# Performance work log

Measured on AMD Instinct MI355X. Metric: run time of the kernel, lower is better.

## Reference

```python
import jax, jax.numpy as jnp
import numpy as np

B = 131072
NF, E = 9, 8
D0 = NF * E  # 72
H = 64       # expert hidden
O = 8        # expert output
T, SE, SH = 3, 3, 3
VOCAB = 160000

PARAM_SHAPES = {
    "emb_table": (VOCAB, E),
    "spec0_W1": (T, SE, D0, H), "spec0_b1": (T, SE, H),
    "spec0_W2": (T, SE, H, O),  "spec0_b2": (T, SE, O),
    "shar0_W1": (SH, D0, H),    "shar0_b1": (SH, H),
    "shar0_W2": (SH, H, O),     "shar0_b2": (SH, O),
    "gate0_W1": (T, D0, H),     "gate0_b1": (T, H),
    "gate0_W2": (T, H, O),      "gate0_b2": (T, O),
    "gate0_W3": (T, O, SE + SH),
    "sgate0_W1": (D0, H), "sgate0_b1": (H,),
    "sgate0_W2": (H, O),  "sgate0_b2": (O,),
    "sgate0_W3": (O, T * SE + SH),
    "spec1_W1": (T, SE, O, H), "spec1_b1": (T, SE, H),
    "spec1_W2": (T, SE, H, O), "spec1_b2": (T, SE, O),
    "shar1_W1": (SH, O, H),    "shar1_b1": (SH, H),
    "shar1_W2": (SH, H, O),    "shar1_b2": (SH, O),
    "gate1_W1": (T, O, H),     "gate1_b1": (T, H),
    "gate1_W2": (T, H, O),     "gate1_b2": (T, O),
    "gate1_W3": (T, O, SE + SH),
    "tower_W": (T, O, 1), "tower_b": (T, 1),
}


def setup_inputs() -> dict:
    key = jax.random.key(0)
    keys = jax.random.split(key, len(PARAM_SHAPES) + 1)
    inp = {n: jax.random.normal(k, s, jnp.float32) * 0.1
           for (n, s), k in zip(PARAM_SHAPES.items(), keys[:-1])}
    inp["cat_idx"] = jax.random.randint(keys[-1], (B, NF), 0, VOCAB, jnp.int32)
    return inp


def _cgc(task_x, shared_x, sW1, sb1, sW2, sb2, hW1, hb1, hW2, hb2,
         gW1, gb1, gW2, gb2, gW3, sgate=None):
    """One CGC level. task_x: [T,B,in], shared_x: [B,in]."""
    # task-specific experts, batched over (task, expert)
    h = jax.nn.relu(jnp.einsum('tbi,teih->tebh', task_x, sW1) + sb1[:, :, None, :])
    spec = jax.nn.relu(jnp.einsum('tebh,teho->tebo', h, sW2) + sb2[:, :, None, :])  # [T,SE,B,O]
    # shared experts, batched over expert
    hs = jax.nn.relu(jnp.einsum('bi,eih->ebh', shared_x, hW1) + hb1[:, None, :])
    shar = jax.nn.relu(jnp.einsum('ebh,eho->ebo', hs, hW2) + hb2[:, None, :])       # [SH,B,O]
    # per-task gates: MLP[64,8] relu -> linear(no bias) -> softmax over SE+SH experts
    g = jax.nn.relu(jnp.einsum('tbi,tih->tbh', task_x, gW1) + gb1[:, None, :])
    g = jax.nn.relu(jnp.einsum('tbh,tho->tbo', g, gW2) + gb2[:, None, :])
    gw = jax.nn.softmax(jnp.einsum('tbo,toe->tbe', g, gW3), axis=-1)                # [T,B,SE+SH]
    experts = jnp.concatenate(
        [spec, jnp.broadcast_to(shar[None], (spec.shape[0],) + shar.shape)], axis=1)  # [T,SE+SH,B,O]
    task_out = jnp.einsum('tebo,tbe->tbo', experts, gw)                             # [T,B,O]
    if sgate is None:
        return task_out, None
    sgW1, sgb1, sgW2, sgb2, sgW3 = sgate
    gs = jax.nn.relu(shared_x @ sgW1 + sgb1)
    gs = jax.nn.relu(gs @ sgW2 + sgb2)
    gws = jax.nn.softmax(gs @ sgW3, axis=-1)                                        # [B,T*SE+SH]
    all_e = jnp.concatenate([spec.reshape(T * SE, spec.shape[2], O), shar], axis=0)  # [T*SE+SH,B,O]
    shared_out = jnp.einsum('ebo,be->bo', all_e, gws)
    return task_out, shared_out


def _forward(cat_idx, p):
    x = p["emb_table"][cat_idx].reshape(cat_idx.shape[0], -1)  # [B, 72]
    task_x = jnp.broadcast_to(x[None], (T,) + x.shape)
    task_x, shared_x = _cgc(
        task_x, x,
        p["spec0_W1"], p["spec0_b1"], p["spec0_W2"], p["spec0_b2"],
        p["shar0_W1"], p["shar0_b1"], p["shar0_W2"], p["shar0_b2"],
        p["gate0_W1"], p["gate0_b1"], p["gate0_W2"], p["gate0_b2"], p["gate0_W3"],
        sgate=(p["sgate0_W1"], p["sgate0_b1"], p["sgate0_W2"], p["sgate0_b2"], p["sgate0_W3"]))
    task_x, _ = _cgc(
        task_x, shared_x,
        p["spec1_W1"], p["spec1_b1"], p["spec1_W2"], p["spec1_b2"],
        p["shar1_W1"], p["shar1_b1"], p["shar1_W2"], p["shar1_b2"],
        p["gate1_W1"], p["gate1_b1"], p["gate1_W2"], p["gate1_b2"], p["gate1_W3"],
        sgate=None)
    # 3 sigmoid towers -> stacked [T, B, 1] (== dict task_0..task_2 in original)
    out = jax.nn.sigmoid(jnp.einsum('tbo,tok->tbk', task_x, p["tower_W"]) + p["tower_b"][:, None, :])
    return out


def reference(cat_idx, emb_table, spec0_W1, spec0_b1, spec0_W2, spec0_b2,
              shar0_W1, shar0_b1, shar0_W2, shar0_b2,
              gate0_W1, gate0_b1, gate0_W2, gate0_b2, gate0_W3,
              sgate0_W1, sgate0_b1, sgate0_W2, sgate0_b2, sgate0_W3,
              spec1_W1, spec1_b1, spec1_W2, spec1_b2,
              shar1_W1, shar1_b1, shar1_W2, shar1_b2,
              gate1_W1, gate1_b1, gate1_W2, gate1_b2, gate1_W3,
              tower_W, tower_b):
    p = dict(locals())
    p.pop('cat_idx')
    return _forward(cat_idx, p)
```

## Files before the change

### kernel.cpp

```cpp
#include <hip/hip_runtime.h>


#define NT 256
#define EPB 64

typedef unsigned short u16;
typedef unsigned int u32;
typedef __fp16 hv2 __attribute__((ext_vector_type(2)));
typedef __fp16 half8 __attribute__((ext_vector_type(8)));
typedef __attribute__((ext_vector_type(4))) float floatx4;

__device__ __forceinline__ u32 pkh2(float a, float b){
  hv2 v = __builtin_amdgcn_cvt_pkrtz(a, b);
  u32 r; __builtin_memcpy(&r, &v, 4); return r;
}
__device__ __forceinline__ u16 f2h(float a){
  __fp16 h = (__fp16)a; u16 r; __builtin_memcpy(&r, &h, 2); return r;
}
__device__ __forceinline__ float h2f(u16 v){
  __fp16 h; __builtin_memcpy(&h, &v, 2); return (float)h;
}
__device__ __forceinline__ float dot2(u32 a, u32 b, float c){
  hv2 av, bv; __builtin_memcpy(&av, &a, 4); __builtin_memcpy(&bv, &b, 4);
  return __builtin_amdgcn_fdot2(av, bv, c, false);
}

#define W1F0 0
#define W2F0 49152
#define W1F1 57344
#define W2F1 72704
#define OFF_b1P0 80384
#define OFF_b2P0 81408
#define OFF_b1P1 81664
#define OFF_b2P1 82624
#define OFF_G0W3 82864
#define OFF_SG0W3 83008
#define OFF_G1W3 83104
#define OFF_TW   83248
#define OFF_Tb   83272
#define CVT_TOTAL 83275

struct PSrc { const float* p[33]; };

__global__ void cvt_kernel(PSrc S, u32* __restrict__ wsU, float* __restrict__ wsF){
  int i = blockIdx.x*256 + threadIdx.x;
  if (i >= CVT_TOTAL) return;
  if (i < 49152){
    int j2 = i & 3, l = (i>>2)&63, tt = (i>>8)&3;
    int rest = i >> 10; int s = rest % 3, u = rest / 3;
    int k0 = s*32 + (l>>4)*8 + 2*j2;
    int h  = tt*16 + (l&15);
    const float* src = (u<9)  ? S.p[0]  + (u*72)*64
                     : (u<12) ? S.p[4]  + ((u-9)*72)*64
                     : (u<15) ? S.p[8]  + ((u-12)*72)*64
                              : S.p[13];
    float lo = (k0   < 72) ? src[(k0  )*64 + h] : 0.f;
    float hi = (k0+1 < 72) ? src[(k0+1)*64 + h] : 0.f;
    wsU[i] = pkh2(lo, hi);
    return;
  }
  i -= 49152;
  if (i < 8192){
    int j2 = i & 3, l = (i>>2)&63, ks = (i>>8)&1, u = i>>9;
    int q = l >> 4, n = l & 15;
    int h0 = (2*ks + ((2*j2)>>2))*16 + q*4 + ((2*j2)&3);
    const float* src = (u<9)  ? S.p[2]  + u*512
                     : (u<12) ? S.p[6]  + (u-9)*512
                     : (u<15) ? S.p[10] + (u-12)*512
                              : S.p[15];
    float lo = (n<8) ? src[h0*8 + n] : 0.f;
    float hi = (n<8) ? src[(h0+1)*8 + n] : 0.f;
    wsU[W2F0 + i] = pkh2(lo, hi);
    return;
  }
  i -= 8192;
  if (i < 15360){
    int j2 = i & 3, l = (i>>2)&63, tt = (i>>8)&3, u = i>>10;
    int k0 = (l>>4)*8 + 2*j2;
    int n = tt*16 + (l&15);
    const float* src = (u<9) ? S.p[18] + (u*8)*64
                     : (u<12) ? S.p[22] + ((u-9)*8)*64
                              : S.p[26] + ((u-12)*8)*64;
    float lo = (k0   < 8) ? src[(k0  )*64 + n] : 0.f;
    float hi = (k0+1 < 8) ? src[(k0+1)*64 + n] : 0.f;
    wsU[W1F1 + i] = pkh2(lo, hi);
    return;
  }
  i -= 15360;
  if (i < 7680){
    int j2 = i & 3, l = (i>>2)&63, ks = (i>>8)&1, u = i>>9;
    int q = l >> 4, n = l & 15;
    int h0 = (2*ks + ((2*j2)>>2))*16 + q*4 + ((2*j2)&3);
    const float* src = (u<9) ? S.p[20] + u*512
                     : (u<12) ? S.p[24] + (u-9)*512
                              : S.p[28] + (u-12)*512;
    float lo = (n<8) ? src[h0*8 + n] : 0.f;
    float hi = (n<8) ? src[(h0+1)*8 + n] : 0.f;
    wsU[W2F1 + i] = pkh2(lo, hi);
    return;
  }
  i -= 7680;
  if (i < 1024){
    int u = i>>6;
    const float* src = (u<9) ? S.p[1]+u*64 : (u<12) ? S.p[5]+(u-9)*64
                     : (u<15) ? S.p[9]+(u-12)*64 : S.p[14];
    wsF[OFF_b1P0 + i] = src[i&63];
    return;
  }
  i -= 1024;
  if (i < 256){
    int u = i>>4, n = i&15;
    const float* src = (u<9) ? S.p[3]+u*8 : (u<12) ? S.p[7]+(u-9)*8
                     : (u<15) ? S.p[11]+(u-12)*8 : S.p[16];
    wsF[OFF_b2P0 + i] = (n<8) ? src[n] : 0.f;
    return;
  }
  i -= 256;
  if (i < 960){
    int u = i>>6;
    const float* src = (u<9) ? S.p[19]+u*64 : (u<12) ? S.p[23]+(u-9)*64
                               : S.p[27]+(u-12)*64;
    wsF[OFF_b1P1 + i] = src[i&63];
    return;
  }
  i -= 960;
  if (i < 240){
    int u = i>>4, n = i&15;
    const float* src = (u<9) ? S.p[21]+u*8 : (u<12) ? S.p[25]+(u-9)*8
                               : S.p[29]+(u-12)*8;
    wsF[OFF_b2P1 + i] = (n<8) ? src[n] : 0.f;
    return;
  }
  i -= 240;
  if (i < 144){ wsF[OFF_G0W3 + i] = S.p[12][i]; return; }
  i -= 144;
  if (i < 96){ wsF[OFF_SG0W3 + i] = S.p[17][i]; return; }
  i -= 96;
  if (i < 144){ wsF[OFF_G1W3 + i] = S.p[30][i]; return; }
  i -= 144;
  if (i < 24){ wsF[OFF_TW + i] = S.p[31][i]; return; }
  i -= 24;
  wsF[OFF_Tb + i] = S.p[32][i];
}

template<int N>
__device__ __forceinline__ void softmaxT(float (&v)[N]){
  float m = v[0];
  #pragma unroll
  for (int i=1;i<N;i++) m = fmaxf(m, v[i]);
  float s = 0.f;
  #pragma unroll
  for (int i=0;i<N;i++){ v[i] = __expf(v[i]-m); s += v[i]; }
  float inv = 1.f/s;
  #pragma unroll
  for (int i=0;i<N;i++) v[i] *= inv;
}

__global__ __launch_bounds__(NT, 4) void ple_kernel(
    const float* __restrict__ emb, const int* __restrict__ cat,
    const u32* __restrict__ wsU, const float* __restrict__ P,
    float* __restrict__ out, int Btot)
{
  __shared__ u32 S_[7680];
  u32* xsA = S_;
  u32* obT = S_ + 3328;
  const int tid = threadIdx.x;
  const int e = tid & 63;
  const int su = __builtin_amdgcn_readfirstlane(tid >> 6);
  const int lane = tid & 63;
  const int q = lane >> 4;
  const int c16 = lane & 15;
  const int shw_e = ((e>>2)&1)*4;

  {
    const int eg = blockIdx.x*EPB + e;
    auto ldf = [&](int f){
      int idx = cat[eg*9 + f];
      const float* ep = emb + (long)idx*8;
      float4 a = *(const float4*)ep;
      float4 b = *(const float4*)(ep+4);
      uint4 w; w.x = pkh2(a.x,a.y); w.y = pkh2(a.z,a.w);
      w.z = pkh2(b.x,b.y); w.w = pkh2(b.z,b.w);
      *(uint4*)(xsA + e*52 + f*4) = w;
    };
    ldf(su); ldf(su+4);
    if (su == 0) ldf(8);
    *(uint4*)(xsA + e*52 + 36 + su*4) = (uint4){0,0,0,0};
  }
  __syncthreads();

  u16* obp = (u16*)obT;
  const int sh16_q = ((q&1) ? 8 : 0);

  {
    #pragma unroll 1
    for (int k4 = 0; k4 < 4; k4++){
      const int u = su*4 + k4;
      half8 bf[3][4];
      #pragma unroll
      for (int s=0;s<3;s++)
        #pragma unroll
        for (int t=0;t<4;t++)
          bf[s][t] = *(const half8*)(wsU + W1F0 + (((u*3+s)*4+t)*64 + lane)*4);
      floatx4 bias[4];
      #pragma unroll
      for (int t=0;t<4;t++){
        float4 b4 = *(const float4*)(P + OFF_b1P0 + u*64 + t*16 + q*4);
        bias[t] = (floatx4){b4.x, b4.y, b4.z, b4.w};
      }
      const float ob2 = P[OFF_b2P0 + u*16 + c16];
      half8 w2f[2];
      #pragma unroll
      for (int ks=0;ks<2;ks++)
        w2f[ks] = *(const half8*)(wsU + W2F0 + ((u*2+ks)*64 + lane)*4);

      #pragma unroll 1
      for (int m=0;m<4;m++){
        half8 af[3];
        #pragma unroll
        for (int s=0;s<3;s++)
          af[s] = *(const half8*)(xsA + (m*16 + c16)*52 + s*16 + q*4);
        floatx4 acc[4];
        #pragma unroll
        for (int t=0;t<4;t++) acc[t] = bias[t];
        #pragma unroll
        for (int s=0;s<3;s++)
          #pragma unroll
          for (int t=0;t<4;t++)
            acc[t] = __builtin_amdgcn_mfma_f32_16x16x32_f16(bf[s][t], af[s], acc[t], 0,0,0);
        floatx4 oc = (floatx4){ob2, ob2, ob2, ob2};
        #pragma unroll
        for (int ks=0;ks<2;ks++){
          u32 aw[4];
          aw[0] = pkh2(fmaxf(acc[2*ks  ][0],0.f), fmaxf(acc[2*ks  ][1],0.f));
          aw[1] = pkh2(fmaxf(acc[2*ks  ][2],0.f), fmaxf(acc[2*ks  ][3],0.f));
          aw[2] = pkh2(fmaxf(acc[2*ks+1][0],0.f), fmaxf(acc[2*ks+1][1],0.f));
          aw[3] = pkh2(fmaxf(acc[2*ks+1][2],0.f), fmaxf(acc[2*ks+1][3],0.f));
          half8 haf; __builtin_memcpy(&haf, aw, 16);
          oc = __builtin_amdgcn_mfma_f32_16x16x32_f16(haf, w2f[ks], oc, 0,0,0);
        }
        if (c16 < 8){
          #pragma unroll
          for (int r=0;r<4;r++)
            obp[(m*16 + q*4 + r)*136 + sh16_q + c16*16 + u] = f2h(fmaxf(oc[r], 0.f));
        }
      }
    }
  }
  __syncthreads();

  u32* l1in = xsA;
  *(uint4*)(l1in + e*36 + 16 + su*4) = (uint4){0,0,0,0};
  {
    float wv[12];
    {
      const int ug = (su<3) ? 12+su : 15;
      float g8[8];
      #pragma unroll
      for (int j=0;j<8;j++) g8[j] = h2f(obp[e*136 + 2*shw_e + j*16 + ug]);
      if (su < 3){
        float lg[6];
        #pragma unroll
        for (int m=0;m<6;m++){
          float s = 0.f;
          #pragma unroll
          for (int j=0;j<8;j++) s = fmaf(g8[j], P[OFF_G0W3 + su*48 + j*6 + m], s);
          lg[m] = s;
        }
        softmaxT<6>(lg);
        #pragma unroll
        for (int k=0;k<12;k++)
          wv[k] = (k<9) ? (((k/3)==su) ? lg[k%3] : 0.f) : lg[k-6];
      } else {
        float lw[12];
        #pragma unroll
        for (int m=0;m<12;m++){
          float s = 0.f;
          #pragma unroll
          for (int j=0;j<8;j++) s = fmaf(g8[j], P[OFF_SG0W3 + j*12 + m], s);
          lw[m] = s;
        }
        softmaxT<12>(lw);
        #pragma unroll
        for (int k=0;k<12;k++) wv[k] = lw[k];
      }
    }
    u32 wp[6];
    #pragma unroll
    for (int p=0;p<6;p++) wp[p] = pkh2(wv[2*p], wv[2*p+1]);
    float in8[8];
    #pragma unroll
    for (int n=0;n<8;n++){
      const u32* rowp = obT + e*68 + shw_e + n*8;
      uint4 A = *(const uint4*)rowp;
      uint2 Bv = *(const uint2*)(rowp + 4);
      float s = dot2(A.x, wp[0], 0.f);
      s = dot2(A.y, wp[1], s);
      s = dot2(A.z, wp[2], s);
      s = dot2(A.w, wp[3], s);
      s = dot2(Bv.x, wp[4], s);
      s = dot2(Bv.y, wp[5], s);
      in8[n] = s;
    }
    const int dst = (su<3) ? su*4 : 12;
    uint4 lw4; lw4.x = pkh2(in8[0],in8[1]); lw4.y = pkh2(in8[2],in8[3]);
    lw4.z = pkh2(in8[4],in8[5]); lw4.w = pkh2(in8[6],in8[7]);
    *(uint4*)(l1in + e*36 + dst) = lw4;
  }
  __syncthreads();

  {
    #pragma unroll 1
    for (int k4=0;k4<4;k4++){
      const int u = su*4 + k4;
      if (u >= 15) break;
      const int base_u = (u<9) ? (u/3)*4 : ((u<12) ? 12 : (u-12)*4);
      const int aoff = (q==0) ? base_u : (16 + q*4);
      half8 bf1[4];
      #pragma unroll
      for (int t=0;t<4;t++)
        bf1[t] = *(const half8*)(wsU + W1F1 + ((u*4+t)*64 + lane)*4);
      floatx4 bias[4];
      #pragma unroll
      for (int t=0;t<4;t++){
        float4 b4 = *(const float4*)(P + OFF_b1P1 + u*64 + t*16 + q*4);
        bias[t] = (floatx4){b4.x, b4.y, b4.z, b4.w};
      }
      const float ob2 = P[OFF_b2P1 + u*16 + c16];
      half8 w2f[2];
      #pragma unroll
      for (int ks=0;ks<2;ks++)
        w2f[ks] = *(const half8*)(wsU + W2F1 + ((u*2+ks)*64 + lane)*4);

      #pragma unroll 1
      for (int m=0;m<4;m++){
        half8 af = *(const half8*)(l1in + (m*16 + c16)*36 + aoff);
        floatx4 acc[4];
        #pragma unroll
        for (int t=0;t<4;t++) acc[t] = bias[t];
        #pragma unroll
        for (int t=0;t<4;t++)
          acc[t] = __builtin_amdgcn_mfma_f32_16x16x32_f16(bf1[t], af, acc[t], 0,0,0);
        floatx4 oc = (floatx4){ob2, ob2, ob2, ob2};
        #pragma unroll
        for (int ks=0;ks<2;ks++){
          u32 aw[4];
          aw[0] = pkh2(fmaxf(acc[2*ks  ][0],0.f), fmaxf(acc[2*ks  ][1],0.f));
          aw[1] = pkh2(fmaxf(acc[2*ks  ][2],0.f), fmaxf(acc[2*ks  ][3],0.f));
          aw[2] = pkh2(fmaxf(acc[2*ks+1][0],0.f), fmaxf(acc[2*ks+1][1],0.f));
          aw[3] = pkh2(fmaxf(acc[2*ks+1][2],0.f), fmaxf(acc[2*ks+1][3],0.f));
          half8 haf; __builtin_memcpy(&haf, aw, 16);
          oc = __builtin_amdgcn_mfma_f32_16x16x32_f16(haf, w2f[ks], oc, 0,0,0);
        }
        if (c16 < 8){
          #pragma unroll
          for (int r=0;r<4;r++)
            obp[(m*16 + q*4 + r)*136 + sh16_q + c16*16 + u] = f2h(fmaxf(oc[r], 0.f));
        }
      }
    }
  }
  __syncthreads();

  if (su < 3){
    const int t = su;
    float g8[8];
    #pragma unroll
    for (int j=0;j<8;j++) g8[j] = h2f(obp[e*136 + 2*shw_e + j*16 + 12+t]);
    float lg[6];
    #pragma unroll
    for (int m=0;m<6;m++){
      float s = 0.f;
      #pragma unroll
      for (int j=0;j<8;j++) s = fmaf(g8[j], P[OFF_G1W3 + t*48 + j*6 + m], s);
      lg[m] = s;
    }
    softmaxT<6>(lg);
    float wv[12];
    #pragma unroll
    for (int k=0;k<12;k++)
      wv[k] = (k<9) ? (((k/3)==t) ? lg[k%3] : 0.f) : lg[k-6];
    u32 wp[6];
    #pragma unroll
    for (int p=0;p<6;p++) wp[p] = pkh2(wv[2*p], wv[2*p+1]);
    float s = P[OFF_Tb + t];
    #pragma unroll
    for (int n=0;n<8;n++){
      const u32* rowp = obT + e*68 + shw_e + n*8;
      uint4 A = *(const uint4*)rowp;
      uint2 Bv = *(const uint2*)(rowp + 4);
      float v = dot2(A.x, wp[0], 0.f);
      v = dot2(A.y, wp[1], v);
      v = dot2(A.z, wp[2], v);
      v = dot2(A.w, wp[3], v);
      v = dot2(Bv.x, wp[4], v);
      v = dot2(Bv.y, wp[5], v);
      s = fmaf(v, P[OFF_TW + t*8 + n], s);
    }
    out[t*Btot + blockIdx.x*EPB + e] = 1.f/(1.f + __expf(-s));
  }
}

extern "C" void kernel_launch(void* const* d_in, const int* in_sizes, int n_in,
                              void* d_out, int out_size, void* d_ws, size_t ws_size,
                              hipStream_t stream)
{
  const float* emb = (const float*)d_in[0];
  const int* cat = (const int*)d_in[34];
  float* out = (float*)d_out;
  u32* wsU = (u32*)d_ws;
  float* wsF = (float*)d_ws;
  PSrc S;
  for (int k=0;k<33;k++) S.p[k] = (const float*)d_in[k+1];
  const int B = in_sizes[34] / 9;

  cvt_kernel<<<(CVT_TOTAL+255)/256, 256, 0, stream>>>(S, wsU, wsF);
  ple_kernel<<<B/EPB, NT, 0, stream>>>(emb, cat, wsU, wsF, out, B);
}
```

Before: 181.8 us.

## Transpose expert-output LDS layout and mix experts with packed fp16 FMAs

The second MFMA now runs with swapped operands, so each lane holds four consecutive output features of one sample. These are written to LDS as one packed uint2 per lane instead of four scattered 16-bit stores. Gate inputs and expert outputs are then read back as contiguous uint4 rows, and the gated mixture is accumulated with packed half2 FMAs per expert instead of per-feature dot2 chains. Tower weights are pre-packed to fp16 pairs so the tower can use dot2. Accumulating the mixture in fp16 rather than fp32 costs some precision.

```diff
diff --git a/kernel.cpp b/kernel.cpp
--- a/kernel.cpp
+++ b/kernel.cpp
@@ -14,15 +14,19 @@
   hv2 v = __builtin_amdgcn_cvt_pkrtz(a, b);
   u32 r; __builtin_memcpy(&r, &v, 4); return r;
 }
-__device__ __forceinline__ u16 f2h(float a){
-  __fp16 h = (__fp16)a; u16 r; __builtin_memcpy(&r, &h, 2); return r;
-}
 __device__ __forceinline__ float h2f(u16 v){
   __fp16 h; __builtin_memcpy(&h, &v, 2); return (float)h;
 }
+__device__ __forceinline__ hv2 u2h(u32 w){ hv2 v; __builtin_memcpy(&v, &w, 4); return v; }
+__device__ __forceinline__ u32 h2u(hv2 v){ u32 w; __builtin_memcpy(&w, &v, 4); return w; }
 __device__ __forceinline__ float dot2(u32 a, u32 b, float c){
-  hv2 av, bv; __builtin_memcpy(&av, &a, 4); __builtin_memcpy(&bv, &b, 4);
-  return __builtin_amdgcn_fdot2(av, bv, c, false);
+  return __builtin_amdgcn_fdot2(u2h(a), u2h(b), c, false);
+}
+__device__ __forceinline__ void unp8(uint4 gw, float g8[8]){
+  g8[0]=h2f((u16)(gw.x&0xffffu)); g8[1]=h2f((u16)(gw.x>>16));
+  g8[2]=h2f((u16)(gw.y&0xffffu)); g8[3]=h2f((u16)(gw.y>>16));
+  g8[4]=h2f((u16)(gw.z&0xffffu)); g8[5]=h2f((u16)(gw.z>>16));
+  g8[6]=h2f((u16)(gw.w&0xffffu)); g8[7]=h2f((u16)(gw.w>>16));
 }
 
 #define W1F0 0
@@ -38,7 +42,8 @@
 #define OFF_G1W3 83104
 #define OFF_TW   83248
 #define OFF_Tb   83272
-#define CVT_TOTAL 83275
+#define OFF_TWH  83275
+#define CVT_TOTAL 83287
 
 struct PSrc { const float* p[33]; };
 
@@ -140,7 +145,12 @@
   i -= 144;
   if (i < 24){ wsF[OFF_TW + i] = S.p[31][i]; return; }
   i -= 24;
-  wsF[OFF_Tb + i] = S.p[32][i];
+  if (i < 3){ wsF[OFF_Tb + i] = S.p[32][i]; return; }
+  i -= 3;
+  {
+    int t = i>>2, w = i&3;
+    wsU[OFF_TWH + i] = pkh2(S.p[31][t*8 + 2*w], S.p[31][t*8 + 2*w + 1]);
+  }
 }
 
 template<int N>
@@ -170,7 +180,6 @@
   const int lane = tid & 63;
   const int q = lane >> 4;
   const int c16 = lane & 15;
-  const int shw_e = ((e>>2)&1)*4;
 
   {
     const int eg = blockIdx.x*EPB + e;
@@ -189,9 +198,6 @@
   }
   __syncthreads();
 
-  u16* obp = (u16*)obT;
-  const int sh16_q = ((q&1) ? 8 : 0);
-
   {
     #pragma unroll 1
     for (int k4 = 0; k4 < 4; k4++){
@@ -208,7 +214,7 @@
         float4 b4 = *(const float4*)(P + OFF_b1P0 + u*64 + t*16 + q*4);
         bias[t] = (floatx4){b4.x, b4.y, b4.z, b4.w};
       }
-      const float ob2 = P[OFF_b2P0 + u*16 + c16];
+      float4 b2v = *(const float4*)(P + OFF_b2P0 + u*16 + q*4);
       half8 w2f[2];
       #pragma unroll
       for (int ks=0;ks<2;ks++)
@@ -228,7 +234,7 @@
           #pragma unroll
           for (int t=0;t<4;t++)
             acc[t] = __builtin_amdgcn_mfma_f32_16x16x32_f16(bf[s][t], af[s], acc[t], 0,0,0);
-        floatx4 oc = (floatx4){ob2, ob2, ob2, ob2};
+        floatx4 oc = (floatx4){b2v.x, b2v.y, b2v.z, b2v.w};
         #pragma unroll
         for (int ks=0;ks<2;ks++){
           u32 aw[4];
@@ -237,12 +243,13 @@
           aw[2] = pkh2(fmaxf(acc[2*ks+1][0],0.f), fmaxf(acc[2*ks+1][1],0.f));
           aw[3] = pkh2(fmaxf(acc[2*ks+1][2],0.f), fmaxf(acc[2*ks+1][3],0.f));
           half8 haf; __builtin_memcpy(&haf, aw, 16);
-          oc = __builtin_amdgcn_mfma_f32_16x16x32_f16(haf, w2f[ks], oc, 0,0,0);
-        }
-        if (c16 < 8){
-          #pragma unroll
-          for (int r=0;r<4;r++)
-            obp[(m*16 + q*4 + r)*136 + sh16_q + c16*16 + u] = f2h(fmaxf(oc[r], 0.f));
+          oc = __builtin_amdgcn_mfma_f32_16x16x32_f16(w2f[ks], haf, oc, 0,0,0);
+        }
+        if (q < 2){
+          uint2 ov;
+          ov.x = pkh2(fmaxf(oc[0],0.f), fmaxf(oc[1],0.f));
+          ov.y = pkh2(fmaxf(oc[2],0.f), fmaxf(oc[3],0.f));
+          *(uint2*)(obT + (m*16 + c16)*68 + u*4 + q*2) = ov;
         }
       }
     }
@@ -255,9 +262,8 @@
     float wv[12];
     {
       const int ug = (su<3) ? 12+su : 15;
-      float g8[8];
-      #pragma unroll
-      for (int j=0;j<8;j++) g8[j] = h2f(obp[e*136 + 2*shw_e + j*16 + ug]);
+      uint4 gw = *(const uint4*)(obT + e*68 + ug*4);
+      float g8[8]; unp8(gw, g8);
       if (su < 3){
         float lg[6];
         #pragma unroll
@@ -285,26 +291,20 @@
         for (int k=0;k<12;k++) wv[k] = lw[k];
       }
     }
-    u32 wp[6];
+    hv2 a01 = (hv2){0,0}, a23 = (hv2){0,0}, a45 = (hv2){0,0}, a67 = (hv2){0,0};
     #pragma unroll
-    for (int p=0;p<6;p++) wp[p] = pkh2(wv[2*p], wv[2*p+1]);
-    float in8[8];
-    #pragma unroll
-    for (int n=0;n<8;n++){
-      const u32* rowp = obT + e*68 + shw_e + n*8;
-      uint4 A = *(const uint4*)rowp;
-      uint2 Bv = *(const uint2*)(rowp + 4);
-      float s = dot2(A.x, wp[0], 0.f);
-      s = dot2(A.y, wp[1], s);
-      s = dot2(A.z, wp[2], s);
-      s = dot2(A.w, wp[3], s);
-      s = dot2(Bv.x, wp[4], s);
-      s = dot2(Bv.y, wp[5], s);
-      in8[n] = s;
+    for (int u=0;u<12;u++){
+      uint4 ow = *(const uint4*)(obT + e*68 + u*4);
+      __fp16 wh = (__fp16)wv[u];
+      hv2 wp = (hv2){wh, wh};
+      a01 = u2h(ow.x)*wp + a01;
+      a23 = u2h(ow.y)*wp + a23;
+      a45 = u2h(ow.z)*wp + a45;
+      a67 = u2h(ow.w)*wp + a67;
     }
     const int dst = (su<3) ? su*4 : 12;
-    uint4 lw4; lw4.x = pkh2(in8[0],in8[1]); lw4.y = pkh2(in8[2],in8[3]);
-    lw4.z = pkh2(in8[4],in8[5]); lw4.w = pkh2(in8[6],in8[7]);
+    uint4 lw4; lw4.x = h2u(a01); lw4.y = h2u(a23);
+    lw4.z = h2u(a45); lw4.w = h2u(a67);
     *(uint4*)(l1in + e*36 + dst) = lw4;
   }
   __syncthreads();
@@ -326,7 +326,7 @@
         float4 b4 = *(const float4*)(P + OFF_b1P1 + u*64 + t*16 + q*4);
         bias[t] = (floatx4){b4.x, b4.y, b4.z, b4.w};
       }
-      const float ob2 = P[OFF_b2P1 + u*16 + c16];
+      float4 b2v = *(const float4*)(P + OFF_b2P1 + u*16 + q*4);
       half8 w2f[2];
       #pragma unroll
       for (int ks=0;ks<2;ks++)
@@ -341,7 +341,7 @@
         #pragma unroll
         for (int t=0;t<4;t++)
           acc[t] = __builtin_amdgcn_mfma_f32_16x16x32_f16(bf1[t], af, acc[t], 0,0,0);
-        floatx4 oc = (floatx4){ob2, ob2, ob2, ob2};
+        floatx4 oc = (floatx4){b2v.x, b2v.y, b2v.z, b2v.w};
         #pragma unroll
         for (int ks=0;ks<2;ks++){
           u32 aw[4];
@@ -350,12 +350,13 @@
           aw[2] = pkh2(fmaxf(acc[2*ks+1][0],0.f), fmaxf(acc[2*ks+1][1],0.f));
           aw[3] = pkh2(fmaxf(acc[2*ks+1][2],0.f), fmaxf(acc[2*ks+1][3],0.f));
           half8 haf; __builtin_memcpy(&haf, aw, 16);
-          oc = __builtin_amdgcn_mfma_f32_16x16x32_f16(haf, w2f[ks], oc, 0,0,0);
-        }
-        if (c16 < 8){
-          #pragma unroll
-          for (int r=0;r<4;r++)
-            obp[(m*16 + q*4 + r)*136 + sh16_q + c16*16 + u] = f2h(fmaxf(oc[r], 0.f));
+          oc = __builtin_amdgcn_mfma_f32_16x16x32_f16(w2f[ks], haf, oc, 0,0,0);
+        }
+        if (q < 2){
+          uint2 ov;
+          ov.x = pkh2(fmaxf(oc[0],0.f), fmaxf(oc[1],0.f));
+          ov.y = pkh2(fmaxf(oc[2],0.f), fmaxf(oc[3],0.f));
+          *(uint2*)(obT + (m*16 + c16)*68 + u*4 + q*2) = ov;
         }
       }
     }
@@ -364,9 +365,8 @@
 
   if (su < 3){
     const int t = su;
-    float g8[8];
-    #pragma unroll
-    for (int j=0;j<8;j++) g8[j] = h2f(obp[e*136 + 2*shw_e + j*16 + 12+t]);
+    uint4 gw = *(const uint4*)(obT + e*68 + (12+t)*4);
+    float g8[8]; unp8(gw, g8);
     float lg[6];
     #pragma unroll
     for (int m=0;m<6;m++){
@@ -380,23 +380,22 @@
     #pragma unroll
     for (int k=0;k<12;k++)
       wv[k] = (k<9) ? (((k/3)==t) ? lg[k%3] : 0.f) : lg[k-6];
-    u32 wp[6];
+    hv2 a01 = (hv2){0,0}, a23 = (hv2){0,0}, a45 = (hv2){0,0}, a67 = (hv2){0,0};
     #pragma unroll
-    for (int p=0;p<6;p++) wp[p] = pkh2(wv[2*p], wv[2*p+1]);
+    for (int u=0;u<12;u++){
+      uint4 ow = *(const uint4*)(obT + e*68 + u*4);
+      __fp16 wh = (__fp16)wv[u];
+      hv2 wp = (hv2){wh, wh};
+      a01 = u2h(ow.x)*wp + a01;
+      a23 = u2h(ow.y)*wp + a23;
+      a45 = u2h(ow.z)*wp + a45;
+      a67 = u2h(ow.w)*wp + a67;
+    }
     float s = P[OFF_Tb + t];
-    #pragma unroll
-    for (int n=0;n<8;n++){
-      const u32* rowp = obT + e*68 + shw_e + n*8;
-      uint4 A = *(const uint4*)rowp;
-      uint2 Bv = *(const uint2*)(rowp + 4);
-      float v = dot2(A.x, wp[0], 0.f);
-      v = dot2(A.y, wp[1], v);
-      v = dot2(A.z, wp[2], v);
-      v = dot2(A.w, wp[3], v);
-      v = dot2(Bv.x, wp[4], v);
-      v = dot2(Bv.y, wp[5], v);
-      s = fmaf(v, P[OFF_TW + t*8 + n], s);
-    }
+    s = dot2(h2u(a01), wsU[OFF_TWH + t*4 + 0], s);
+    s = dot2(h2u(a23), wsU[OFF_TWH + t*4 + 1], s);
+    s = dot2(h2u(a45), wsU[OFF_TWH + t*4 + 2], s);
+    s = dot2(h2u(a67), wsU[OFF_TWH + t*4 + 3], s);
     out[t*Btot + blockIdx.x*EPB + e] = 1.f/(1.f + __expf(-s));
   }
 }
```

New measurement: 177.6 us. 1.02x faster.
